# Kernel tuning notes

Hardware: AMD Instinct MI355X
Metric: run time of the kernel (lower is better)

Reference implementation:

```python
import jax, jax.numpy as jnp
import numpy as np

B, T, C = 4, 2048, 2048
N_HEAD = 16
HEAD_DIM = C // N_HEAD
ROPE_BASE = 10000.0


def setup_inputs() -> dict:
    key = jax.random.key(0)
    k1, k2, k3 = jax.random.split(key, 3)
    x = jax.random.normal(k1, (B, T, C), dtype=jnp.float32)
    Wqkv = jax.random.normal(k2, (C, 3 * C), dtype=jnp.float32) * 0.02
    bqkv = jnp.zeros((3 * C,), dtype=jnp.float32)
    Wproj = jax.random.normal(k3, (C, C), dtype=jnp.float32) * 0.02
    bproj = jnp.zeros((C,), dtype=jnp.float32)
    return {"x": x, "Wqkv": Wqkv, "bqkv": bqkv, "Wproj": Wproj, "bproj": bproj}


def _rope_cos_sin(seq_len, head_dim, dtype):
    inv_freq = 1.0 / (ROPE_BASE ** (jnp.arange(0, head_dim, 2, dtype=jnp.float32) / head_dim))
    t = jnp.arange(seq_len, dtype=jnp.float32)
    freqs = jnp.einsum("i,j->ij", t, inv_freq)          # [T, D/2]
    emb = jnp.concatenate([freqs, freqs], axis=-1)       # [T, D]
    return jnp.cos(emb).astype(dtype), jnp.sin(emb).astype(dtype)


def _rotate_half(x):
    half = x.shape[-1] // 2
    x1, x2 = x[..., :half], x[..., half:]
    return jnp.concatenate([-x2, x1], axis=-1)


def reference(x, Wqkv, bqkv, Wproj, bproj):
    b, t, c = x.shape
    qkv = x @ Wqkv + bqkv                                # [B, T, 3C]
    q, k, v = jnp.split(qkv, 3, axis=-1)
    # [B, T, C] -> [B, H, T, D]
    def to_heads(u):
        return u.reshape(b, t, N_HEAD, HEAD_DIM).transpose(0, 2, 1, 3)
    q, k, v = to_heads(q), to_heads(k), to_heads(v)
    cos, sin = _rope_cos_sin(t, HEAD_DIM, x.dtype)       # [T, D]
    cos = cos[None, None]                                # [1, 1, T, D]
    sin = sin[None, None]
    q = q * cos + _rotate_half(q) * sin
    k = k * cos + _rotate_half(k) * sin
    scale = 1.0 / np.sqrt(HEAD_DIM).astype(np.float32)
    scores = jnp.einsum("bhqd,bhkd->bhqk", q, k) * scale  # [B, H, T, T]
    causal = jnp.tril(jnp.ones((t, t), dtype=bool))
    scores = jnp.where(causal[None, None], scores, jnp.finfo(scores.dtype).min)
    att = jax.nn.softmax(scores, axis=-1)
    y = jnp.einsum("bhqk,bhkd->bhqd", att, v)             # [B, H, T, D]
    y = y.transpose(0, 2, 1, 3).reshape(b, t, c)
    return y @ Wproj + bproj
```

## Files before the change

### kernel.cpp

```cpp
#include <hip/hip_runtime.h>
#include <hip/hip_bf16.h>
#include <stdint.h>
#include <math.h>

#define NB 4
#define NT 2048
#define NC 2048
#define NH 16
#define HD 128
#define BT (NB*NT)

typedef __attribute__((ext_vector_type(8))) short s16x8;
typedef __attribute__((ext_vector_type(4))) short s16x4;
typedef __attribute__((ext_vector_type(4))) float f32x4;

typedef __attribute__((address_space(1))) void as1_void;
typedef __attribute__((address_space(3))) void as3_void;

static __device__ __forceinline__ unsigned short f2bf(float f) {
  union { float f; uint32_t u; } v; v.f = f;
  return (unsigned short)((v.u + 0x7fffu + ((v.u >> 16) & 1u)) >> 16);
}
static __device__ __forceinline__ float bf2f(unsigned short u) {
  union { uint32_t u; float f; } v; v.u = ((uint32_t)u) << 16;
  return v.f;
}
static __device__ __forceinline__ void async16(unsigned short* lds, const unsigned short* g) {
  __builtin_amdgcn_global_load_lds((as1_void*)g, (as3_void*)lds, 16, 0, 0);
}
static __device__ __forceinline__ uint32_t lds_off(void* p) {
  return (uint32_t)(size_t)(as3_void*)p;
}

__global__ void k_convert_bf16(const float* __restrict__ in, unsigned short* __restrict__ out, int n8) {
  int i = blockIdx.x * blockDim.x + threadIdx.x;
  if (i >= n8) return;
  const float4* p = (const float4*)in + (size_t)i * 2;
  float4 a = p[0], b = p[1];
  union { unsigned short s[8]; uint4 u; } o;
  o.s[0] = f2bf(a.x); o.s[1] = f2bf(a.y); o.s[2] = f2bf(a.z); o.s[3] = f2bf(a.w);
  o.s[4] = f2bf(b.x); o.s[5] = f2bf(b.y); o.s[6] = f2bf(b.z); o.s[7] = f2bf(b.w);
  ((uint4*)out)[i] = o.u;
}

__global__ void k_transpose_bf16(const float* __restrict__ W, unsigned short* __restrict__ WT, int K, int N) {
  __shared__ unsigned short tile[64][65];
  const int k0 = blockIdx.y * 64, n0 = blockIdx.x * 64;
  const int t = threadIdx.x;
  const int jj = t & 63, base_i = t >> 6;
  #pragma unroll
  for (int p = 0; p < 16; ++p) {
    int i = p * 4 + base_i;
    tile[i][jj] = f2bf(W[(size_t)(k0 + i) * N + n0 + jj]);
  }
  __syncthreads();
  #pragma unroll
  for (int p = 0; p < 16; ++p) {
    int j = p * 4 + base_i;
    WT[(size_t)(n0 + j) * K + k0 + jj] = tile[jj][j];
  }
}

__global__ void k_rope(unsigned short* __restrict__ Q, unsigned short* __restrict__ Kb) {
  int idx = blockIdx.x * 256 + threadIdx.x;
  int g = idx & 7;
  int tpos = (idx >> 3) & (NT - 1);
  int bh = idx >> 14;
  size_t o = ((size_t)bh * NT + tpos) * HD + g * 8;
  s16x8 qlo = *(const s16x8*)(Q + o),  qhi = *(const s16x8*)(Q + o + 64);
  s16x8 klo = *(const s16x8*)(Kb + o), khi = *(const s16x8*)(Kb + o + 64);
  s16x8 oql, oqh, okl, okh;
  const float qs = 0.08838834764831845f * 1.4426950408889634f;
  #pragma unroll
  for (int e = 0; e < 8; ++e) {
    const int d = g * 8 + e;
    float invf = exp2f(-(float)d * 0.2076205059304602f);
    float ang = (float)tpos * invf;
    float s, c;
    __sincosf(ang, &s, &c);
    float q1 = bf2f((unsigned short)qlo[e]), q2 = bf2f((unsigned short)qhi[e]);
    float k1 = bf2f((unsigned short)klo[e]), k2 = bf2f((unsigned short)khi[e]);
    oql[e] = (short)f2bf((q1 * c - q2 * s) * qs);
    oqh[e] = (short)f2bf((q2 * c + q1 * s) * qs);
    okl[e] = (short)f2bf(k1 * c - k2 * s);
    okh[e] = (short)f2bf(k2 * c + k1 * s);
  }
  *(s16x8*)(Q + o)       = oql;
  *(s16x8*)(Q + o + 64)  = oqh;
  *(s16x8*)(Kb + o)      = okl;
  *(s16x8*)(Kb + o + 64) = okh;
}

template<int MODE>
__global__ __launch_bounds__(256, 2)
void k_gemm_bt2(const unsigned short* __restrict__ A,
                const unsigned short* __restrict__ Bt,
                const float* __restrict__ bias,
                float* __restrict__ OutF,
                unsigned short* __restrict__ Qd,
                unsigned short* __restrict__ Kd,
                unsigned short* __restrict__ Vd,
                int M, int N, int K)
{
  __shared__ __align__(16) unsigned short Al[256 * 64];
  __shared__ __align__(16) unsigned short Bl[128 * 64];
  const int t = threadIdx.x;
  const int l = t & 63;
  const int wv = t >> 6;
  const int wm = wv >> 1, wn = wv & 1;
  const int bm = blockIdx.y * 256, bn = blockIdx.x * 128;
  const int lr = l & 15, lg = l >> 4;

  f32x4 acc[8][4];
  #pragma unroll
  for (int i = 0; i < 8; ++i)
    #pragma unroll
    for (int j = 0; j < 4; ++j)
      acc[i][j] = f32x4{0.f, 0.f, 0.f, 0.f};

  for (int k0 = 0; k0 < K; k0 += 64) {
    #pragma unroll
    for (int i = 0; i < 8; ++i) {
      const int Cc = i * 256 + t;
      const int row = Cc >> 3;
      const int kc = (Cc & 7) ^ (row & 7);
      async16(&Al[(i * 256 + (t & 192)) * 8], &A[(size_t)(bm + row) * K + k0 + kc * 8]);
    }
    #pragma unroll
    for (int i = 0; i < 4; ++i) {
      const int Cc = i * 256 + t;
      const int row = Cc >> 3;
      const int kc = (Cc & 7) ^ (row & 7);
      async16(&Bl[(i * 256 + (t & 192)) * 8], &Bt[(size_t)(bn + row) * K + k0 + kc * 8]);
    }
    __syncthreads();
    #pragma unroll
    for (int kk = 0; kk < 2; ++kk) {
      s16x8 af[8], bfr[4];
      #pragma unroll
      for (int mi = 0; mi < 8; ++mi) {
        const int row = wm * 128 + mi * 16 + lr;
        const int ch = (kk * 4 + lg) ^ (row & 7);
        af[mi] = *(const s16x8*)&Al[row * 64 + ch * 8];
      }
      #pragma unroll
      for (int ni = 0; ni < 4; ++ni) {
        const int row = wn * 64 + ni * 16 + lr;
        const int ch = (kk * 4 + lg) ^ (row & 7);
        bfr[ni] = *(const s16x8*)&Bl[row * 64 + ch * 8];
      }
      __builtin_amdgcn_s_setprio(1);
      #pragma unroll
      for (int mi = 0; mi < 8; ++mi)
        #pragma unroll
        for (int ni = 0; ni < 4; ++ni)
          acc[mi][ni] = __builtin_amdgcn_mfma_f32_16x16x32_bf16(af[mi], bfr[ni], acc[mi][ni], 0, 0, 0);
      __builtin_amdgcn_s_setprio(0);
    }
    __syncthreads();
  }

  #pragma unroll
  for (int mi = 0; mi < 8; ++mi) {
    #pragma unroll
    for (int ni = 0; ni < 4; ++ni) {
      const int col = bn + wn * 64 + ni * 16 + lr;
      const float bv = bias[col];
      #pragma unroll
      for (int r = 0; r < 4; ++r) {
        const int row = bm + wm * 128 + mi * 16 + lg * 4 + r;
        const float v = acc[mi][ni][r] + bv;
        if (MODE == 1) {
          OutF[(size_t)row * N + col] = v;
        } else {
          const int which = col >> 11;
          const int cc = col & 2047;
          const int h = cc >> 7, d = cc & 127;
          const int b = row >> 11, tp = row & 2047;
          unsigned short* dst = (which == 0) ? Qd : (which == 1 ? Kd : Vd);
          dst[(((size_t)(b * NH + h)) * NT + tp) * HD + d] = f2bf(v);
        }
      }
    }
  }
}

__global__ __launch_bounds__(256, 2)
void k_attn(const unsigned short* __restrict__ Q,
            const unsigned short* __restrict__ Kg,
            const unsigned short* __restrict__ Vg,
            unsigned short* __restrict__ Yatt)
{
  __shared__ __align__(16) unsigned short Kl[2][64 * 128];
  __shared__ __align__(16) unsigned short Vl[2][64 * 128];
  const int bh = blockIdx.x;
  const int pair = blockIdx.y;
  const int b = bh >> 4, h = bh & 15;
  const int t = threadIdx.x, l = t & 63, wv = t >> 6;
  const int lr = l & 15, lg = l >> 4;
  const size_t hoff = (size_t)bh * NT * HD;
  const unsigned short* Qh = Q + hoff;
  const unsigned short* Kh = Kg + hoff;
  const unsigned short* Vh = Vg + hoff;
  const uint32_t vbase0 = lds_off(&Vl[0][0]);

  auto stageKV = [&](int buf, int kv0) {
    #pragma unroll
    for (int i = 0; i < 4; ++i) {
      const int Cc = i * 256 + t;
      {
        const int krow = Cc >> 4;
        const int kc = (Cc & 15) ^ (krow & 7);
        async16(&Kl[buf][(i * 256 + (t & 192)) * 8], &Kh[(size_t)(kv0 + krow) * HD + kc * 8]);
      }
      {
        const int S = Cc >> 3, c8 = Cc & 7;
        const int kq = S >> 3, dq = S & 7;
        const int vk = kq * 4 + (c8 >> 1), vd = dq * 16 + (c8 & 1) * 8;
        async16(&Vl[buf][(i * 256 + (t & 192)) * 8], &Vh[(size_t)(kv0 + vk) * HD + vd]);
      }
    }
  };

  #pragma unroll 1
  for (int rep = 0; rep < 2; ++rep) {
    const int qb16 = rep ? (15 - pair) : pair;
    const int q0w = qb16 * 128 + wv * 32;
    const int qrowA = q0w + lr, qrowB = q0w + 16 + lr;

    __syncthreads();

    s16x8 qfA[4], qfB[4];
    #pragma unroll
    for (int m = 0; m < 4; ++m) {
      qfA[m] = *(const s16x8*)(Qh + (size_t)qrowA * HD + m * 32 + lg * 8);
      qfB[m] = *(const s16x8*)(Qh + (size_t)qrowB * HD + m * 32 + lg * 8);
    }

    f32x4 ytA[8], ytB[8];
    #pragma unroll
    for (int n = 0; n < 8; ++n) { ytA[n] = f32x4{0.f,0.f,0.f,0.f}; ytB[n] = f32x4{0.f,0.f,0.f,0.f}; }
    float mrunA = -1e30f, lrunA = 0.f, mrunB = -1e30f, lrunB = 0.f;

    auto computeTile = [&](int buf, int kv0) {
      f32x4 stA[4], stB[4];
      __builtin_amdgcn_s_setprio(1);
      #pragma unroll
      for (int kt = 0; kt < 4; ++kt) {
        f32x4 a = f32x4{0.f,0.f,0.f,0.f}, bq = f32x4{0.f,0.f,0.f,0.f};
        const int krow = kt * 16 + lr;
        #pragma unroll
        for (int m = 0; m < 4; ++m) {
          const int ch = (m * 4 + lg) ^ (krow & 7);
          s16x8 kf = *(const s16x8*)&Kl[buf][krow * 128 + ch * 8];
          a  = __builtin_amdgcn_mfma_f32_16x16x32_bf16(kf, qfA[m], a, 0, 0, 0);
          bq = __builtin_amdgcn_mfma_f32_16x16x32_bf16(kf, qfB[m], bq, 0, 0, 0);
        }
        stA[kt] = a; stB[kt] = bq;
      }
      __builtin_amdgcn_s_setprio(0);

      if (kv0 + 63 > q0w) {
        #pragma unroll
        for (int kt = 0; kt < 4; ++kt)
          #pragma unroll
          for (int r = 0; r < 4; ++r) {
            const int key = kv0 + kt * 16 + lg * 4 + r;
            if (key > qrowA) stA[kt][r] = -3.0e38f;
            if (key > qrowB) stB[kt][r] = -3.0e38f;
          }
      }

      float tmA = -3.0e38f, tmB = -3.0e38f;
      #pragma unroll
      for (int kt = 0; kt < 4; ++kt)
        #pragma unroll
        for (int r = 0; r < 4; ++r) { tmA = fmaxf(tmA, stA[kt][r]); tmB = fmaxf(tmB, stB[kt][r]); }
      tmA = fmaxf(tmA, __shfl_xor(tmA, 16)); tmA = fmaxf(tmA, __shfl_xor(tmA, 32));
      tmB = fmaxf(tmB, __shfl_xor(tmB, 16)); tmB = fmaxf(tmB, __shfl_xor(tmB, 32));
      if (!__all((tmA - mrunA <= 8.0f) && (tmB - mrunB <= 8.0f))) {
        const float mnA = fmaxf(mrunA, tmA), mnB = fmaxf(mrunB, tmB);
        const float fsA = exp2f(mrunA - mnA), fsB = exp2f(mrunB - mnB);
        mrunA = mnA; mrunB = mnB;
        lrunA *= fsA; lrunB *= fsB;
        #pragma unroll
        for (int n = 0; n < 8; ++n)
          #pragma unroll
          for (int r = 0; r < 4; ++r) { ytA[n][r] *= fsA; ytB[n][r] *= fsB; }
      }

      float pvA[16], pvB[16];
      float psA = 0.f, psB = 0.f;
      #pragma unroll
      for (int kt = 0; kt < 4; ++kt)
        #pragma unroll
        for (int r = 0; r < 4; ++r) {
          const float pa = exp2f(stA[kt][r] - mrunA);
          const float pb = exp2f(stB[kt][r] - mrunB);
          psA += pa; psB += pb;
          pvA[kt * 4 + r] = pa; pvB[kt * 4 + r] = pb;
        }
      lrunA += psA; lrunB += psB;

      union { uint32_t w[4]; s16x8 v; } puA[2], puB[2];
      #pragma unroll
      for (int gk = 0; gk < 2; ++gk)
        #pragma unroll
        for (int w = 0; w < 4; ++w) {
          const int i0 = (gk * 2 + (w >> 1)) * 4 + (w & 1) * 2;
          asm("v_cvt_pk_bf16_f32 %0, %1, %2" : "=v"(puA[gk].w[w]) : "v"(pvA[i0]), "v"(pvA[i0 + 1]));
          asm("v_cvt_pk_bf16_f32 %0, %1, %2" : "=v"(puB[gk].w[w]) : "v"(pvB[i0]), "v"(pvB[i0 + 1]));
        }

      const uint32_t vb = vbase0 + (uint32_t)buf * 16384;
      #pragma unroll
      for (int gk = 0; gk < 2; ++gk) {
        s16x4 va[8], vb2[8];
        #pragma unroll
        for (int n = 0; n < 8; ++n) {
          const uint32_t a0 = vb + ((uint32_t)((gk * 8 + lg) * 8 + n)) * 128 + (uint32_t)lr * 8;
          asm volatile("ds_read_b64_tr_b16 %0, %1" : "=v"(va[n])  : "v"(a0));
          asm volatile("ds_read_b64_tr_b16 %0, %1" : "=v"(vb2[n]) : "v"(a0 + 4096));
        }
        asm volatile("s_waitcnt lgkmcnt(0)" ::: "memory");
        __builtin_amdgcn_sched_barrier(0);
        __builtin_amdgcn_s_setprio(1);
        #pragma unroll
        for (int n = 0; n < 8; ++n) {
          s16x8 vf;
          vf[0] = va[n][0];  vf[1] = va[n][1];  vf[2] = va[n][2];  vf[3] = va[n][3];
          vf[4] = vb2[n][0]; vf[5] = vb2[n][1]; vf[6] = vb2[n][2]; vf[7] = vb2[n][3];
          ytA[n] = __builtin_amdgcn_mfma_f32_16x16x32_bf16(vf, puA[gk].v, ytA[n], 0, 0, 0);
          ytB[n] = __builtin_amdgcn_mfma_f32_16x16x32_bf16(vf, puB[gk].v, ytB[n], 0, 0, 0);
        }
        __builtin_amdgcn_s_setprio(0);
      }
    };

    const int nkv = 2 * qb16 + 2;
    stageKV(0, 0);
    asm volatile("s_waitcnt vmcnt(0)" ::: "memory");
    __syncthreads();
    int buf = 0;
    #pragma unroll 1
    for (int kv = 0; kv < nkv - 1; ++kv) {
      stageKV(buf ^ 1, (kv + 1) * 64);
      computeTile(buf, kv * 64);
      asm volatile("s_waitcnt vmcnt(0)" ::: "memory");
      __builtin_amdgcn_s_barrier();
      buf ^= 1;
    }
    if ((nkv - 1) * 64 <= q0w + 31)
      computeTile(buf, (nkv - 1) * 64);

    lrunA += __shfl_xor(lrunA, 16); lrunA += __shfl_xor(lrunA, 32);
    lrunB += __shfl_xor(lrunB, 16); lrunB += __shfl_xor(lrunB, 32);
    const float invA = 1.f / lrunA, invB = 1.f / lrunB;
    unsigned short* yrowA = Yatt + (size_t)(b * NT + qrowA) * NC + h * HD;
    unsigned short* yrowB = Yatt + (size_t)(b * NT + qrowB) * NC + h * HD;
    #pragma unroll
    for (int n = 0; n < 8; ++n) {
      uint32_t u0, u1;
      asm("v_cvt_pk_bf16_f32 %0, %1, %2" : "=v"(u0) : "v"(ytA[n][0] * invA), "v"(ytA[n][1] * invA));
      asm("v_cvt_pk_bf16_f32 %0, %1, %2" : "=v"(u1) : "v"(ytA[n][2] * invA), "v"(ytA[n][3] * invA));
      uint2 pk; pk.x = u0; pk.y = u1;
      *(uint2*)(yrowA + n * 16 + lg * 4) = pk;
      asm("v_cvt_pk_bf16_f32 %0, %1, %2" : "=v"(u0) : "v"(ytB[n][0] * invB), "v"(ytB[n][1] * invB));
      asm("v_cvt_pk_bf16_f32 %0, %1, %2" : "=v"(u1) : "v"(ytB[n][2] * invB), "v"(ytB[n][3] * invB));
      pk.x = u0; pk.y = u1;
      *(uint2*)(yrowB + n * 16 + lg * 4) = pk;
    }
  }
}

extern "C" void kernel_launch(void* const* d_in, const int* in_sizes, int n_in,
                              void* d_out, int out_size, void* d_ws, size_t ws_size,
                              hipStream_t stream) {
  (void)in_sizes; (void)n_in; (void)out_size; (void)ws_size;
  const float* x     = (const float*)d_in[0];
  const float* Wqkv  = (const float*)d_in[1];
  const float* bqkv  = (const float*)d_in[2];
  const float* Wproj = (const float*)d_in[3];
  const float* bproj = (const float*)d_in[4];
  float* out = (float*)d_out;
  char* ws = (char*)d_ws;

  unsigned short* xb     = (unsigned short*)(ws);
  unsigned short* WqkvT  = (unsigned short*)(ws + 33554432);
  unsigned short* WprojT = (unsigned short*)(ws + 58720256);
  unsigned short* Qb     = (unsigned short*)(ws + 67108864);
  unsigned short* Kb     = (unsigned short*)(ws + 100663296);
  unsigned short* Vb     = (unsigned short*)(ws + 134217728);
  unsigned short* att    = xb;

  k_convert_bf16<<<dim3(8192), dim3(256), 0, stream>>>(x, xb, BT * NC / 8);
  k_transpose_bf16<<<dim3(96, 32), dim3(256), 0, stream>>>(Wqkv, WqkvT, NC, 3 * NC);
  k_transpose_bf16<<<dim3(32, 32), dim3(256), 0, stream>>>(Wproj, WprojT, NC, NC);
  k_gemm_bt2<0><<<dim3(48, 32), dim3(256), 0, stream>>>(xb, WqkvT, bqkv, nullptr, Qb, Kb, Vb, BT, 3 * NC, NC);
  k_rope<<<dim3(4096), dim3(256), 0, stream>>>(Qb, Kb);
  k_attn<<<dim3(64, 8), dim3(256), 0, stream>>>(Qb, Kb, Vb, att);
  k_gemm_bt2<1><<<dim3(16, 32), dim3(256), 0, stream>>>(att, WprojT, bproj, out, nullptr, nullptr, nullptr, BT, NC, NC);
}
```

Measured before the change: 408.6 us.

## Fuse RoPE into QKV GEMM epilogue via LDS exchange between wave halves

Removes the separate RoPE kernel and applies the rotary embedding and query scaling inside the QKV GEMM epilogue. Each Q/K head tile spans 128 columns across two waves, so the waves swap their accumulator halves through shared memory to pair d with d+64 before rotating. This avoids a full extra read and write of Q and K plus a kernel launch. In exchange the epilogue gains extra synchronization, LDS traffic and sincos work.

```diff
diff --git a/kernel.cpp b/kernel.cpp
--- a/kernel.cpp
+++ b/kernel.cpp
@@ -59,36 +59,6 @@
     int j = p * 4 + base_i;
     WT[(size_t)(n0 + j) * K + k0 + jj] = tile[jj][j];
   }
-}
-
-__global__ void k_rope(unsigned short* __restrict__ Q, unsigned short* __restrict__ Kb) {
-  int idx = blockIdx.x * 256 + threadIdx.x;
-  int g = idx & 7;
-  int tpos = (idx >> 3) & (NT - 1);
-  int bh = idx >> 14;
-  size_t o = ((size_t)bh * NT + tpos) * HD + g * 8;
-  s16x8 qlo = *(const s16x8*)(Q + o),  qhi = *(const s16x8*)(Q + o + 64);
-  s16x8 klo = *(const s16x8*)(Kb + o), khi = *(const s16x8*)(Kb + o + 64);
-  s16x8 oql, oqh, okl, okh;
-  const float qs = 0.08838834764831845f * 1.4426950408889634f;
-  #pragma unroll
-  for (int e = 0; e < 8; ++e) {
-    const int d = g * 8 + e;
-    float invf = exp2f(-(float)d * 0.2076205059304602f);
-    float ang = (float)tpos * invf;
-    float s, c;
-    __sincosf(ang, &s, &c);
-    float q1 = bf2f((unsigned short)qlo[e]), q2 = bf2f((unsigned short)qhi[e]);
-    float k1 = bf2f((unsigned short)klo[e]), k2 = bf2f((unsigned short)khi[e]);
-    oql[e] = (short)f2bf((q1 * c - q2 * s) * qs);
-    oqh[e] = (short)f2bf((q2 * c + q1 * s) * qs);
-    okl[e] = (short)f2bf(k1 * c - k2 * s);
-    okh[e] = (short)f2bf(k2 * c + k1 * s);
-  }
-  *(s16x8*)(Q + o)       = oql;
-  *(s16x8*)(Q + o + 64)  = oqh;
-  *(s16x8*)(Kb + o)      = okl;
-  *(s16x8*)(Kb + o + 64) = okh;
 }
 
 template<int MODE>
@@ -160,26 +130,78 @@
     __syncthreads();
   }
 
-  #pragma unroll
-  for (int mi = 0; mi < 8; ++mi) {
-    #pragma unroll
-    for (int ni = 0; ni < 4; ++ni) {
-      const int col = bn + wn * 64 + ni * 16 + lr;
-      const float bv = bias[col];
-      #pragma unroll
-      for (int r = 0; r < 4; ++r) {
-        const int row = bm + wm * 128 + mi * 16 + lg * 4 + r;
-        const float v = acc[mi][ni][r] + bv;
-        if (MODE == 1) {
-          OutF[(size_t)row * N + col] = v;
-        } else {
-          const int which = col >> 11;
-          const int cc = col & 2047;
-          const int h = cc >> 7, d = cc & 127;
-          const int b = row >> 11, tp = row & 2047;
-          unsigned short* dst = (which == 0) ? Qd : (which == 1 ? Kd : Vd);
-          dst[(((size_t)(b * NH + h)) * NT + tp) * HD + d] = f2bf(v);
-        }
+  if (MODE == 1) {
+    #pragma unroll
+    for (int mi = 0; mi < 8; ++mi) {
+      #pragma unroll
+      for (int ni = 0; ni < 4; ++ni) {
+        const int col = bn + wn * 64 + ni * 16 + lr;
+        const float bv = bias[col];
+        #pragma unroll
+        for (int r = 0; r < 4; ++r) {
+          const int row = bm + wm * 128 + mi * 16 + lg * 4 + r;
+          OutF[(size_t)row * N + col] = acc[mi][ni][r] + bv;
+        }
+      }
+    }
+  } else {
+    const int whichB = bn >> 11;
+    const int bb = bm >> 11;
+    const int h = (bn & 2047) >> 7;
+    unsigned short* dst = (whichB == 0) ? Qd : (whichB == 1 ? Kd : Vd);
+    if (whichB == 2) {
+      #pragma unroll
+      for (int mi = 0; mi < 8; ++mi) {
+        #pragma unroll
+        for (int ni = 0; ni < 4; ++ni) {
+          const int col = bn + wn * 64 + ni * 16 + lr;
+          const float bv = bias[col];
+          const int d = wn * 64 + ni * 16 + lr;
+          #pragma unroll
+          for (int r = 0; r < 4; ++r) {
+            const int tp = (bm + wm * 128 + mi * 16 + lg * 4 + r) & 2047;
+            dst[(((size_t)(bb * NH + h)) * NT + tp) * HD + d] = f2bf(acc[mi][ni][r] + bv);
+          }
+        }
+      }
+    } else {
+      const float qsc = (whichB == 0) ? (0.08838834764831845f * 1.4426950408889634f) : 1.0f;
+      float invf[4];
+      #pragma unroll
+      for (int ni = 0; ni < 4; ++ni)
+        invf[ni] = exp2f(-(float)(ni * 16 + lr) * 0.2076205059304602f);
+      float* Ex = (float*)Al;
+      #pragma unroll
+      for (int mc = 0; mc < 4; ++mc) {
+        __syncthreads();
+        #pragma unroll
+        for (int dm = 0; dm < 2; ++dm)
+          #pragma unroll
+          for (int ni = 0; ni < 4; ++ni) {
+            const float bv = bias[bn + wn * 64 + ni * 16 + lr];
+            #pragma unroll
+            for (int r = 0; r < 4; ++r)
+              Ex[(dm * 16 + ni * 4 + r) * 256 + wv * 64 + l] = acc[mc * 2 + dm][ni][r] + bv;
+          }
+        __syncthreads();
+        #pragma unroll
+        for (int dm = 0; dm < 2; ++dm)
+          #pragma unroll
+          for (int ni = 0; ni < 4; ++ni) {
+            const float bv = bias[bn + wn * 64 + ni * 16 + lr];
+            const int d = wn * 64 + ni * 16 + lr;
+            #pragma unroll
+            for (int r = 0; r < 4; ++r) {
+              const int mi = mc * 2 + dm;
+              const int tp = (bm + wm * 128 + mi * 16 + lg * 4 + r) & 2047;
+              const float own = acc[mi][ni][r] + bv;
+              const float oth = Ex[(dm * 16 + ni * 4 + r) * 256 + (wv ^ 1) * 64 + l];
+              float s, c;
+              __sincosf((float)tp * invf[ni], &s, &c);
+              const float out = ((wn == 0) ? (own * c - oth * s) : (own * c + oth * s)) * qsc;
+              dst[(((size_t)(bb * NH + h)) * NT + tp) * HD + d] = f2bf(out);
+            }
+          }
       }
     }
   }
@@ -397,7 +419,6 @@
   k_transpose_bf16<<<dim3(96, 32), dim3(256), 0, stream>>>(Wqkv, WqkvT, NC, 3 * NC);
   k_transpose_bf16<<<dim3(32, 32), dim3(256), 0, stream>>>(Wproj, WprojT, NC, NC);
   k_gemm_bt2<0><<<dim3(48, 32), dim3(256), 0, stream>>>(xb, WqkvT, bqkv, nullptr, Qb, Kb, Vb, BT, 3 * NC, NC);
-  k_rope<<<dim3(4096), dim3(256), 0, stream>>>(Qb, Kb);
   k_attn<<<dim3(64, 8), dim3(256), 0, stream>>>(Qb, Kb, Vb, att);
   k_gemm_bt2<1><<<dim3(16, 32), dim3(256), 0, stream>>>(att, WprojT, bproj, out, nullptr, nullptr, nullptr, BT, NC, NC);
 }
```

Result: faster. 398.5 us (-2.5%).
